# Kernel optimization log

Measured on AMD Instinct MI355X. Metric: run time of the kernel, lower is better.

Reference implementation:

```python
import jax, jax.numpy as jnp
import numpy as np

N_NODES = 100000

def graph_conv(x, src, dst, W_rel, W_root, b, num_nodes):
    # PyG GraphConv: out_i = lin_rel(sum_{j in N(i)} x_j) + lin_root(x_i)
    agg = jax.ops.segment_sum(x[src], dst, num_segments=num_nodes)  # [N, F_in]
    return agg @ W_rel + x @ W_root + b


def setup_inputs() -> dict:
    key = jax.random.key(0)
    ks = jax.random.split(key, 8)
    z = jax.random.normal(ks[0], (N_NODES, 64), dtype=jnp.float32)
    edge_index = jax.random.randint(ks[1], (2, 1600000), 0, N_NODES, dtype=jnp.int64)
    def glorot(k, fi, fo):
        s = (6.0 / (fi + fo)) ** 0.5
        return jax.random.uniform(k, (fi, fo), dtype=jnp.float32, minval=-s, maxval=s)
    return {
        "z": z,
        "edge_index": edge_index,
        "W_rel1": glorot(ks[2], 64, 32), "W_root1": glorot(ks[3], 64, 32), "b1": jnp.zeros((32,), jnp.float32),
        "W_rel2": glorot(ks[4], 32, 16), "W_root2": glorot(ks[5], 32, 16), "b2": jnp.zeros((16,), jnp.float32),
        "W_rel3": glorot(ks[6], 16, 2), "W_root3": glorot(ks[7], 16, 2), "b3": jnp.zeros((2,), jnp.float32),
    }


def reference(z, edge_index, W_rel1, W_root1, b1, W_rel2, W_root2, b2, W_rel3, W_root3, b3):
    src, dst = edge_index[0], edge_index[1]
    h = graph_conv(z, src, dst, W_rel1, W_root1, b1, N_NODES)
    h = jax.nn.relu(h)
    h = graph_conv(h, src, dst, W_rel2, W_root2, b2, N_NODES)
    h = jax.nn.relu(h)
    h = graph_conv(h, src, dst, W_rel3, W_root3, b3, N_NODES)
    return jax.nn.softmax(h, axis=-1)
```

## Files before the change

kernel.cpp:

```cpp
#include <hip/hip_runtime.h>


#define RNODES 128
#define NB_MAX 1024
#define CH 4096
#define CMAX 512

template <int Fin, int Fout, bool RELU>
__global__ void linear_q2_kernel(const float* __restrict__ x,
                                 const float* __restrict__ Wrel,
                                 const float* __restrict__ Wroot,
                                 const float* __restrict__ bias,
                                 short* __restrict__ t,
                                 float* __restrict__ tscale,
                                 float* __restrict__ acc, int N) {
    const bool rootTask = (blockIdx.y != 0);
    const float* __restrict__ W = rootTask ? Wroot : Wrel;

    int n = blockIdx.x * blockDim.x + threadIdx.x;
    if (n >= N) return;

    float o[Fout];
#pragma unroll
    for (int f = 0; f < Fout; ++f) o[f] = 0.f;

    const float* xr = x + (size_t)n * Fin;
#pragma unroll
    for (int k = 0; k < Fin; k += 4) {
        float4 v = *(const float4*)(xr + k);
        if (RELU) {
            v.x = fmaxf(v.x, 0.f); v.y = fmaxf(v.y, 0.f);
            v.z = fmaxf(v.z, 0.f); v.w = fmaxf(v.w, 0.f);
        }
        const float xv[4] = {v.x, v.y, v.z, v.w};
#pragma unroll
        for (int kk = 0; kk < 4; ++kk) {
            const float* wr = W + (size_t)(k + kk) * Fout;
#pragma unroll
            for (int f = 0; f < Fout; ++f)
                o[f] = fmaf(xv[kk], wr[f], o[f]);
        }
    }

    if (rootTask) {
#pragma unroll
        for (int f = 0; f < Fout; ++f) o[f] += bias[f];
        float* arow = acc + (size_t)n * Fout;
        if constexpr (Fout >= 4) {
#pragma unroll
            for (int f = 0; f < Fout; f += 4)
                *(float4*)(arow + f) = make_float4(o[f], o[f+1], o[f+2], o[f+3]);
        } else {
            *(float2*)arow = make_float2(o[0], o[1]);
        }
    } else {
        float m = 0.f;
#pragma unroll
        for (int f = 0; f < Fout; ++f) m = fmaxf(m, fabsf(o[f]));
        const float inv = (m > 0.f) ? (32767.0f / m) : 0.f;
        tscale[n] = m * (1.0f / 32767.0f);

        short q[Fout];
#pragma unroll
        for (int f = 0; f < Fout; ++f) q[f] = (short)__float2int_rn(o[f] * inv);

        short* trow = t + (size_t)n * Fout;
        if constexpr (Fout >= 8) {
#pragma unroll
            for (int f = 0; f < Fout; f += 8)
                *(int4*)(trow + f) = *(const int4*)(q + f);
        } else {
            *(int*)trow = (int)(unsigned short)q[0] | ((int)q[1] << 16);
        }
    }
}

template <int Fin, int Fout, bool RELU>
__global__ void linear2_kernel(const float* __restrict__ x,
                               const float* __restrict__ Wrel,
                               const float* __restrict__ Wroot,
                               const float* __restrict__ bias,
                               float* __restrict__ t,
                               float* __restrict__ acc, int N) {
    const bool rootTask = (blockIdx.y != 0);
    const float* __restrict__ W = rootTask ? Wroot : Wrel;
    float* __restrict__ outp    = rootTask ? acc : t;

    int n = blockIdx.x * blockDim.x + threadIdx.x;
    if (n >= N) return;

    float o[Fout];
#pragma unroll
    for (int f = 0; f < Fout; ++f) o[f] = 0.f;

    const float* xr = x + (size_t)n * Fin;
#pragma unroll
    for (int k = 0; k < Fin; k += 4) {
        float4 v = *(const float4*)(xr + k);
        if (RELU) {
            v.x = fmaxf(v.x, 0.f); v.y = fmaxf(v.y, 0.f);
            v.z = fmaxf(v.z, 0.f); v.w = fmaxf(v.w, 0.f);
        }
        const float xv[4] = {v.x, v.y, v.z, v.w};
#pragma unroll
        for (int kk = 0; kk < 4; ++kk) {
            const float* wr = W + (size_t)(k + kk) * Fout;
#pragma unroll
            for (int f = 0; f < Fout; ++f)
                o[f] = fmaf(xv[kk], wr[f], o[f]);
        }
    }
    if (rootTask) {
#pragma unroll
        for (int f = 0; f < Fout; ++f) o[f] += bias[f];
    }
    float* op = outp + (size_t)n * Fout;
    if constexpr (Fout >= 4) {
#pragma unroll
        for (int f = 0; f < Fout; f += 4)
            *(float4*)(op + f) = make_float4(o[f], o[f + 1], o[f + 2], o[f + 3]);
    } else {
        *(float2*)op = make_float2(o[0], o[1]);
    }
}

__global__ void hist_chunked_kernel(const int* __restrict__ dst,
                                    int* __restrict__ chunkhist,
                                    int nE, int NB) {
    __shared__ int h[NB_MAX];
    const int c  = blockIdx.x;
    const int e0 = c * CH, e1 = min(e0 + CH, nE);
    for (int b = threadIdx.x; b < NB; b += blockDim.x) h[b] = 0;
    __syncthreads();
    for (int e = e0 + threadIdx.x; e < e1; e += blockDim.x)
        atomicAdd(&h[dst[e] >> 7], 1);
    __syncthreads();
    for (int b = threadIdx.x; b < NB; b += blockDim.x)
        chunkhist[(size_t)c * NB + b] = h[b];
}

__global__ void scan_chunkhist_kernel(int* __restrict__ chunkhist,
                                      int* __restrict__ gtotal,
                                      int C, int NB) {
    __shared__ int s[CMAX];
    const int b = blockIdx.x;
    const int t = threadIdx.x;
    int v = (t < C) ? chunkhist[(size_t)t * NB + b] : 0;
    s[t] = v;
    __syncthreads();
    for (int off = 1; off < CMAX; off <<= 1) {
        int u = (t >= off) ? s[t - off] : 0;
        __syncthreads();
        s[t] += u;
        __syncthreads();
    }
    if (t < C) chunkhist[(size_t)t * NB + b] = s[t] - v;
    if (t == CMAX - 1) gtotal[b] = s[t];
}

__global__ void scan_buckets_kernel(const int* __restrict__ gtotal,
                                    int* __restrict__ bptr, int NB, int nE) {
    __shared__ int s[NB_MAX];
    int t = threadIdx.x;
    int own = (t < NB) ? gtotal[t] : 0;
    s[t] = own;
    __syncthreads();
    for (int off = 1; off < NB_MAX; off <<= 1) {
        int v = (t >= off) ? s[t - off] : 0;
        __syncthreads();
        s[t] += v;
        __syncthreads();
    }
    if (t < NB) bptr[t] = s[t] - own;
    if (t == 0) bptr[NB] = nE;
}

__global__ void bucketize_det_kernel(const int* __restrict__ src,
                                     const int* __restrict__ dst,
                                     const int* __restrict__ chunkpre,
                                     const int* __restrict__ bptr,
                                     unsigned int* __restrict__ records,
                                     int nE, int NB) {
    __shared__ int lcur[NB_MAX];
    const int c  = blockIdx.x;
    const int e0 = c * CH, e1 = min(e0 + CH, nE);
    for (int b = threadIdx.x; b < NB; b += blockDim.x)
        lcur[b] = bptr[b] + chunkpre[(size_t)c * NB + b];
    __syncthreads();
    for (int e = e0 + threadIdx.x; e < e1; e += blockDim.x) {
        int d = dst[e];
        int b = d >> 7;
        int pos = atomicAdd(&lcur[b], 1);
        records[pos] = (unsigned int)src[e] | ((unsigned int)(d & 127) << 17);
    }
}

__global__ void place_merge_kernel(const unsigned int* __restrict__ records,
                                   const int* __restrict__ bptr,
                                   int* __restrict__ rowptr,
                                   int* __restrict__ srcs_sorted,
                                   int N, int nE, int NB) {
    __shared__ int hist[RNODES];
    __shared__ int s[RNODES];
    __shared__ int lcur[RNODES];
    const int b    = blockIdx.x;
    const int base = b * RNODES;
    const int nn   = min(RNODES, N - base);
    const int beg  = bptr[b], end = bptr[b + 1];
    const int t    = threadIdx.x;

    if (t < RNODES) hist[t] = 0;
    __syncthreads();
    for (int i = beg + t; i < end; i += blockDim.x)
        atomicAdd(&hist[records[i] >> 17], 1);
    __syncthreads();

    if (t < RNODES) s[t] = hist[t];
    __syncthreads();
    for (int off = 1; off < RNODES; off <<= 1) {
        int v = (t < RNODES && t >= off) ? s[t - off] : 0;
        __syncthreads();
        if (t < RNODES && t >= off) s[t] += v;
        __syncthreads();
    }
    if (t < nn) {
        int ex = beg + s[t] - hist[t];
        rowptr[base + t] = ex;
        lcur[t] = ex;
    }
    if (b == NB - 1 && t == 0) rowptr[N] = nE;
    __syncthreads();

    for (int i = beg + t; i < end; i += blockDim.x) {
        unsigned int rec = records[i];
        int pos = atomicAdd(&lcur[rec >> 17], 1);
        srcs_sorted[pos] = (int)(rec & 0x1FFFFu);
    }
}

template <int F, bool SOFTMAX>
__global__ void gather_agg_q_kernel(const short* __restrict__ t,
                                    const float* __restrict__ tscale,
                                    const int* __restrict__ rowptr,
                                    const int* __restrict__ srcs,
                                    const float* __restrict__ rootacc,
                                    float* __restrict__ out, int N) {
    constexpr int P = (F >= 4) ? (F / 2) : 1;
    constexpr int S = F / 2;
    int tid = blockIdx.x * blockDim.x + threadIdx.x;
    int n  = (P == 1) ? tid : (tid / P);
    int fp = (P == 1) ? 0   : (tid & (P - 1));
    if (n >= N) return;

    const int* tp = (const int*)t;
    int beg = rowptr[n], end = rowptr[n + 1];
    float sx = 0.f, sy = 0.f;
    int e = beg;
    for (; e + 8 <= end; e += 8) {
        int s[8];
#pragma unroll
        for (int u = 0; u < 8; ++u) s[u] = srcs[e + u];
        int q[8]; float sc[8];
#pragma unroll
        for (int u = 0; u < 8; ++u) {
            q[u]  = tp[s[u] * S + fp];
            sc[u] = tscale[s[u]];
        }
#pragma unroll
        for (int u = 0; u < 8; ++u) {
            float lo = (float)((short)(q[u] & 0xFFFF));
            float hi = (float)(q[u] >> 16);
            sx = fmaf(sc[u], lo, sx);
            sy = fmaf(sc[u], hi, sy);
        }
    }
    for (; e < end; ++e) {
        int s0 = srcs[e];
        int qv = tp[s0 * S + fp];
        float sc = tscale[s0];
        sx = fmaf(sc, (float)((short)(qv & 0xFFFF)), sx);
        sy = fmaf(sc, (float)(qv >> 16), sy);
    }

    const float2 r0 = *(const float2*)(rootacc + (size_t)n * F + 2 * fp);
    float a = r0.x + sx, b = r0.y + sy;
    if (!SOFTMAX) {
        *(float2*)(out + (size_t)n * F + 2 * fp) = make_float2(a, b);
    } else {
        float m = fmaxf(a, b);
        float ea = __expf(a - m), eb = __expf(b - m);
        float inv = 1.0f / (ea + eb);
        *(float2*)(out + (size_t)n * 2) = make_float2(ea * inv, eb * inv);
    }
}

template <int F>
__global__ void scatter_kernel(const float* __restrict__ t,
                               const int* __restrict__ src,
                               const int* __restrict__ dst,
                               float* __restrict__ acc, int nE) {
    int tid = blockIdx.x * blockDim.x + threadIdx.x;
    int e = tid / F;
    if (e >= nE) return;
    int f = tid & (F - 1);
    atomicAdd(acc + (long)dst[e] * F + f, t[(long)src[e] * F + f]);
}

__global__ void softmax2_kernel(const float* __restrict__ h, float* __restrict__ out, int N) {
    int n = blockIdx.x * blockDim.x + threadIdx.x;
    if (n >= N) return;
    float a = h[2 * n], b = h[2 * n + 1];
    float m = fmaxf(a, b);
    float ea = __expf(a - m), eb = __expf(b - m);
    float inv = 1.0f / (ea + eb);
    out[2 * n] = ea * inv;
    out[2 * n + 1] = eb * inv;
}

extern "C" void kernel_launch(void* const* d_in, const int* in_sizes, int n_in,
                              void* d_out, int out_size, void* d_ws, size_t ws_size,
                              hipStream_t stream) {
    const float* z      = (const float*)d_in[0];
    const int*   ei     = (const int*)d_in[1];
    const float* Wrel1  = (const float*)d_in[2];
    const float* Wroot1 = (const float*)d_in[3];
    const float* b1     = (const float*)d_in[4];
    const float* Wrel2  = (const float*)d_in[5];
    const float* Wroot2 = (const float*)d_in[6];
    const float* b2     = (const float*)d_in[7];
    const float* Wrel3  = (const float*)d_in[8];
    const float* Wroot3 = (const float*)d_in[9];
    const float* b3     = (const float*)d_in[10];

    const int N  = in_sizes[0] / 64;
    const int nE = in_sizes[1] / 2;
    const int* src = ei;
    const int* dst = ei + nE;
    const int NB = (N + RNODES - 1) / RNODES;
    const int C  = (nE + CH - 1) / CH;

    char* wsb = (char*)d_ws;
    size_t off = 0;
    auto take = [&](size_t bytes) -> void* {
        void* p = (void*)(wsb + off);
        off = (off + bytes + 255) & ~(size_t)255;
        return p;
    };
    int*          chunkhist   = (int*)take((size_t)CMAX * NB_MAX * 4);
    int*          gtotal      = (int*)take((size_t)NB_MAX * 4);
    int*          bptr        = (int*)take((size_t)(NB_MAX + 1) * 4);
    unsigned int* records     = (unsigned int*)take((size_t)nE * 4);
    int*          rowptr      = (int*)take((size_t)(N + 1) * 4);
    int*          srcs_sorted = (int*)take((size_t)nE * 4);
    short*        t1          = (short*)take((size_t)N * 32 * 2);
    float*        s1          = (float*)take((size_t)N * 4);
    float*        h1          = (float*)take((size_t)N * 32 * 4);
    short*        t2          = (short*)take((size_t)N * 16 * 2);
    float*        s2          = (float*)take((size_t)N * 4);
    float*        h2          = (float*)take((size_t)N * 16 * 4);
    short*        t3          = (short*)take((size_t)N * 2 * 2);
    float*        s3          = (float*)take((size_t)N * 4);
    float*        h3          = (float*)take((size_t)N * 2 * 4);
    const size_t needed = off;

    const int B = 256;
    const int nodeBlocks = (N + B - 1) / B;
    const dim3 linGrid(nodeBlocks, 2);
    const bool packOK = (N <= (1 << 17)) && (NB <= NB_MAX) && (C <= CMAX);

    if (ws_size >= needed && packOK) {
        hist_chunked_kernel<<<C, 512, 0, stream>>>(dst, chunkhist, nE, NB);
        scan_chunkhist_kernel<<<NB, CMAX, 0, stream>>>(chunkhist, gtotal, C, NB);
        scan_buckets_kernel<<<1, NB_MAX, 0, stream>>>(gtotal, bptr, NB, nE);
        bucketize_det_kernel<<<C, 512, 0, stream>>>(src, dst, chunkhist, bptr, records, nE, NB);
        place_merge_kernel<<<NB, 512, 0, stream>>>(records, bptr, rowptr, srcs_sorted, N, nE, NB);

        linear_q2_kernel<64, 32, false><<<linGrid, B, 0, stream>>>(
            z, Wrel1, Wroot1, b1, t1, s1, h1, N);
        gather_agg_q_kernel<32, false><<<((size_t)N * 16 + B - 1) / B, B, 0, stream>>>(
            t1, s1, rowptr, srcs_sorted, h1, h1, N);

        linear_q2_kernel<32, 16, true><<<linGrid, B, 0, stream>>>(
            h1, Wrel2, Wroot2, b2, t2, s2, h2, N);
        gather_agg_q_kernel<16, false><<<((size_t)N * 8 + B - 1) / B, B, 0, stream>>>(
            t2, s2, rowptr, srcs_sorted, h2, h2, N);

        linear_q2_kernel<16, 2, true><<<linGrid, B, 0, stream>>>(
            h2, Wrel3, Wroot3, b3, t3, s3, h3, N);
        gather_agg_q_kernel<2, true><<<((size_t)N + B - 1) / B, B, 0, stream>>>(
            t3, s3, rowptr, srcs_sorted, h3, (float*)d_out, N);
    } else {
        float* regionA = (float*)d_ws;
        float* regionB = regionA + (size_t)N * 32;
        float* ft1 = regionA;
        float* fh1 = regionB;
        float* ft2 = regionA;
        float* fh2 = regionA + (size_t)N * 16;
        float* ft3 = regionB;
        float* fh3 = regionB + (size_t)N * 2;
        linear2_kernel<64, 32, false><<<linGrid, B, 0, stream>>>(z, Wrel1, Wroot1, b1, ft1, fh1, N);
        scatter_kernel<32><<<((size_t)nE * 32 + B - 1) / B, B, 0, stream>>>(ft1, src, dst, fh1, nE);
        linear2_kernel<32, 16, true><<<linGrid, B, 0, stream>>>(fh1, Wrel2, Wroot2, b2, ft2, fh2, N);
        scatter_kernel<16><<<((size_t)nE * 16 + B - 1) / B, B, 0, stream>>>(ft2, src, dst, fh2, nE);
        linear2_kernel<16, 2, true><<<linGrid, B, 0, stream>>>(fh2, Wrel3, Wroot3, b3, ft3, fh3, N);
        scatter_kernel<2><<<((size_t)nE * 2 + B - 1) / B, B, 0, stream>>>(ft3, src, dst, fh3, nE);
        softmax2_kernel<<<nodeBlocks, B, 0, stream>>>(fh3, (float*)d_out, N);
    }
}
```

Baseline: 248.1 us.

## Inline quantization scale into gathered rows for layers 2 and 3

```diff
diff --git a/kernel.cpp b/kernel.cpp
--- a/kernel.cpp
+++ b/kernel.cpp
@@ -58,19 +58,28 @@
 #pragma unroll
         for (int f = 0; f < Fout; ++f) m = fmaxf(m, fabsf(o[f]));
         const float inv = (m > 0.f) ? (32767.0f / m) : 0.f;
-        tscale[n] = m * (1.0f / 32767.0f);
+        const float sc  = m * (1.0f / 32767.0f);
 
         short q[Fout];
 #pragma unroll
         for (int f = 0; f < Fout; ++f) q[f] = (short)__float2int_rn(o[f] * inv);
 
-        short* trow = t + (size_t)n * Fout;
-        if constexpr (Fout >= 8) {
-#pragma unroll
-            for (int f = 0; f < Fout; f += 8)
+        if constexpr (Fout == 32) {
+            tscale[n] = sc;
+            short* trow = t + (size_t)n * 32;
+#pragma unroll
+            for (int f = 0; f < 32; f += 8)
                 *(int4*)(trow + f) = *(const int4*)(q + f);
+        } else if constexpr (Fout == 16) {
+            short* trow = t + (size_t)n * 32;
+            *(int4*)(trow)     = *(const int4*)(q);
+            *(int4*)(trow + 8) = *(const int4*)(q + 8);
+            ((float*)trow)[8]  = sc;
         } else {
-            *(int*)trow = (int)(unsigned short)q[0] | ((int)q[1] << 16);
+            int2 r;
+            r.x = (int)(unsigned short)q[0] | ((int)q[1] << 16);
+            r.y = __float_as_int(sc);
+            *(int2*)(t + (size_t)n * 4) = r;
         }
     }
 }
@@ -287,6 +296,93 @@
     if (!SOFTMAX) {
         *(float2*)(out + (size_t)n * F + 2 * fp) = make_float2(a, b);
     } else {
+        float m = fmaxf(a, b);
+        float ea = __expf(a - m), eb = __expf(b - m);
+        float inv = 1.0f / (ea + eb);
+        *(float2*)(out + (size_t)n * 2) = make_float2(ea * inv, eb * inv);
+    }
+}
+
+__global__ void gather16_inl_kernel(const short* __restrict__ t,
+                                    const int* __restrict__ rowptr,
+                                    const int* __restrict__ srcs,
+                                    const float* __restrict__ rootacc,
+                                    float* __restrict__ out, int N) {
+    int tid = blockIdx.x * blockDim.x + threadIdx.x;
+    int n  = tid >> 3;
+    int fp = tid & 7;
+    if (n >= N) return;
+
+    const int* tp = (const int*)t;
+    int beg = rowptr[n], end = rowptr[n + 1];
+    float sx = 0.f, sy = 0.f;
+    int e = beg;
+    for (; e + 8 <= end; e += 8) {
+        int s[8];
+#pragma unroll
+        for (int u = 0; u < 8; ++u) s[u] = srcs[e + u];
+        int q[8]; float sc[8];
+#pragma unroll
+        for (int u = 0; u < 8; ++u) {
+            const int* row = tp + (size_t)s[u] * 16;
+            q[u]  = row[fp];
+            sc[u] = __int_as_float(row[8]);
+        }
+#pragma unroll
+        for (int u = 0; u < 8; ++u) {
+            sx = fmaf(sc[u], (float)((short)(q[u] & 0xFFFF)), sx);
+            sy = fmaf(sc[u], (float)(q[u] >> 16), sy);
+        }
+    }
+    for (; e < end; ++e) {
+        const int* row = tp + (size_t)srcs[e] * 16;
+        int qv = row[fp];
+        float sc = __int_as_float(row[8]);
+        sx = fmaf(sc, (float)((short)(qv & 0xFFFF)), sx);
+        sy = fmaf(sc, (float)(qv >> 16), sy);
+    }
+
+    const float2 r0 = *(const float2*)(rootacc + (size_t)n * 16 + 2 * fp);
+    *(float2*)(out + (size_t)n * 16 + 2 * fp) = make_float2(r0.x + sx, r0.y + sy);
+}
+
+__global__ void gather2_inl_kernel(const short* __restrict__ t,
+                                   const int* __restrict__ rowptr,
+                                   const int* __restrict__ srcs,
+                                   const float* __restrict__ rootacc,
+                                   float* __restrict__ out, int N) {
+    int tid = blockIdx.x * blockDim.x + threadIdx.x;
+    int n  = tid >> 2;
+    int fp = tid & 3;
+    if (n >= N) return;
+
+    const int2* tp = (const int2*)t;
+    int beg = rowptr[n], end = rowptr[n + 1];
+    float sx = 0.f, sy = 0.f;
+    int e = beg + fp;
+    for (; e + 12 < end; e += 16) {
+        int s0 = srcs[e], s1 = srcs[e + 4], s2 = srcs[e + 8], s3 = srcs[e + 12];
+        int2 r0 = tp[s0], r1 = tp[s1], r2 = tp[s2], r3 = tp[s3];
+        sx = fmaf(__int_as_float(r0.y), (float)((short)(r0.x & 0xFFFF)), sx);
+        sy = fmaf(__int_as_float(r0.y), (float)(r0.x >> 16), sy);
+        sx = fmaf(__int_as_float(r1.y), (float)((short)(r1.x & 0xFFFF)), sx);
+        sy = fmaf(__int_as_float(r1.y), (float)(r1.x >> 16), sy);
+        sx = fmaf(__int_as_float(r2.y), (float)((short)(r2.x & 0xFFFF)), sx);
+        sy = fmaf(__int_as_float(r2.y), (float)(r2.x >> 16), sy);
+        sx = fmaf(__int_as_float(r3.y), (float)((short)(r3.x & 0xFFFF)), sx);
+        sy = fmaf(__int_as_float(r3.y), (float)(r3.x >> 16), sy);
+    }
+    for (; e < end; e += 4) {
+        int2 r = tp[srcs[e]];
+        sx = fmaf(__int_as_float(r.y), (float)((short)(r.x & 0xFFFF)), sx);
+        sy = fmaf(__int_as_float(r.y), (float)(r.x >> 16), sy);
+    }
+    sx += __shfl_xor(sx, 1, 64); sy += __shfl_xor(sy, 1, 64);
+    sx += __shfl_xor(sx, 2, 64); sy += __shfl_xor(sy, 2, 64);
+
+    if (fp == 0) {
+        const float2 r0 = *(const float2*)(rootacc + (size_t)n * 2);
+        float a = r0.x + sx, b = r0.y + sy;
         float m = fmaxf(a, b);
         float ea = __expf(a - m), eb = __expf(b - m);
         float inv = 1.0f / (ea + eb);
@@ -355,11 +451,9 @@
     short*        t1          = (short*)take((size_t)N * 32 * 2);
     float*        s1          = (float*)take((size_t)N * 4);
     float*        h1          = (float*)take((size_t)N * 32 * 4);
-    short*        t2          = (short*)take((size_t)N * 16 * 2);
-    float*        s2          = (float*)take((size_t)N * 4);
+    short*        t2          = (short*)take((size_t)N * 64);
     float*        h2          = (float*)take((size_t)N * 16 * 4);
-    short*        t3          = (short*)take((size_t)N * 2 * 2);
-    float*        s3          = (float*)take((size_t)N * 4);
+    short*        t3          = (short*)take((size_t)N * 8);
     float*        h3          = (float*)take((size_t)N * 2 * 4);
     const size_t needed = off;
 
@@ -381,14 +475,14 @@
             t1, s1, rowptr, srcs_sorted, h1, h1, N);
 
         linear_q2_kernel<32, 16, true><<<linGrid, B, 0, stream>>>(
-            h1, Wrel2, Wroot2, b2, t2, s2, h2, N);
-        gather_agg_q_kernel<16, false><<<((size_t)N * 8 + B - 1) / B, B, 0, stream>>>(
-            t2, s2, rowptr, srcs_sorted, h2, h2, N);
+            h1, Wrel2, Wroot2, b2, t2, nullptr, h2, N);
+        gather16_inl_kernel<<<((size_t)N * 8 + B - 1) / B, B, 0, stream>>>(
+            t2, rowptr, srcs_sorted, h2, h2, N);
 
         linear_q2_kernel<16, 2, true><<<linGrid, B, 0, stream>>>(
-            h2, Wrel3, Wroot3, b3, t3, s3, h3, N);
-        gather_agg_q_kernel<2, true><<<((size_t)N + B - 1) / B, B, 0, stream>>>(
-            t3, s3, rowptr, srcs_sorted, h3, (float*)d_out, N);
+            h2, Wrel3, Wroot3, b3, t3, nullptr, h3, N);
+        gather2_inl_kernel<<<((size_t)N * 4 + B - 1) / B, B, 0, stream>>>(
+            t3, rowptr, srcs_sorted, h3, (float*)d_out, N);
     } else {
         float* regionA = (float*)d_ws;
         float* regionB = regionA + (size_t)N * 32;
```

After: 243.0 us. -2.0%, faster.

## Aggregate directly from dst-bucketed records with shared-memory atomics, drop CSR build

Applied to the files above, without the earlier changes.

```diff
diff --git a/kernel.cpp b/kernel.cpp
--- a/kernel.cpp
+++ b/kernel.cpp
@@ -58,19 +58,28 @@
 #pragma unroll
         for (int f = 0; f < Fout; ++f) m = fmaxf(m, fabsf(o[f]));
         const float inv = (m > 0.f) ? (32767.0f / m) : 0.f;
-        tscale[n] = m * (1.0f / 32767.0f);
+        const float sc  = m * (1.0f / 32767.0f);
 
         short q[Fout];
 #pragma unroll
         for (int f = 0; f < Fout; ++f) q[f] = (short)__float2int_rn(o[f] * inv);
 
-        short* trow = t + (size_t)n * Fout;
-        if constexpr (Fout >= 8) {
-#pragma unroll
-            for (int f = 0; f < Fout; f += 8)
+        if constexpr (Fout == 32) {
+            tscale[n] = sc;
+            short* trow = t + (size_t)n * 32;
+#pragma unroll
+            for (int f = 0; f < 32; f += 8)
                 *(int4*)(trow + f) = *(const int4*)(q + f);
+        } else if constexpr (Fout == 16) {
+            short* trow = t + (size_t)n * 32;
+            *(int4*)(trow)     = *(const int4*)(q);
+            *(int4*)(trow + 8) = *(const int4*)(q + 8);
+            ((float*)trow)[8]  = sc;
         } else {
-            *(int*)trow = (int)(unsigned short)q[0] | ((int)q[1] << 16);
+            int2 r;
+            r.x = (int)(unsigned short)q[0] | ((int)q[1] << 16);
+            r.y = __float_as_int(sc);
+            *(int2*)(t + (size_t)n * 4) = r;
         }
     }
 }
@@ -195,102 +204,80 @@
     }
 }
 
-__global__ void place_merge_kernel(const unsigned int* __restrict__ records,
-                                   const int* __restrict__ bptr,
-                                   int* __restrict__ rowptr,
-                                   int* __restrict__ srcs_sorted,
-                                   int N, int nE, int NB) {
-    __shared__ int hist[RNODES];
-    __shared__ int s[RNODES];
-    __shared__ int lcur[RNODES];
+template <int F, bool SOFTMAX>
+__global__ void bucket_gather_kernel(const short* __restrict__ t,
+                                     const float* __restrict__ tscale,
+                                     const unsigned int* __restrict__ records,
+                                     const int* __restrict__ bptr,
+                                     const float* __restrict__ rootacc,
+                                     float* __restrict__ out, int N) {
+    __shared__ float accs[RNODES * (F + 1)];
     const int b    = blockIdx.x;
     const int base = b * RNODES;
     const int nn   = min(RNODES, N - base);
     const int beg  = bptr[b], end = bptr[b + 1];
-    const int t    = threadIdx.x;
-
-    if (t < RNODES) hist[t] = 0;
-    __syncthreads();
-    for (int i = beg + t; i < end; i += blockDim.x)
-        atomicAdd(&hist[records[i] >> 17], 1);
-    __syncthreads();
-
-    if (t < RNODES) s[t] = hist[t];
-    __syncthreads();
-    for (int off = 1; off < RNODES; off <<= 1) {
-        int v = (t < RNODES && t >= off) ? s[t - off] : 0;
-        __syncthreads();
-        if (t < RNODES && t >= off) s[t] += v;
-        __syncthreads();
-    }
-    if (t < nn) {
-        int ex = beg + s[t] - hist[t];
-        rowptr[base + t] = ex;
-        lcur[t] = ex;
-    }
-    if (b == NB - 1 && t == 0) rowptr[N] = nE;
-    __syncthreads();
-
-    for (int i = beg + t; i < end; i += blockDim.x) {
-        unsigned int rec = records[i];
-        int pos = atomicAdd(&lcur[rec >> 17], 1);
-        srcs_sorted[pos] = (int)(rec & 0x1FFFFu);
-    }
-}
-
-template <int F, bool SOFTMAX>
-__global__ void gather_agg_q_kernel(const short* __restrict__ t,
-                                    const float* __restrict__ tscale,
-                                    const int* __restrict__ rowptr,
-                                    const int* __restrict__ srcs,
-                                    const float* __restrict__ rootacc,
-                                    float* __restrict__ out, int N) {
-    constexpr int P = (F >= 4) ? (F / 2) : 1;
-    constexpr int S = F / 2;
-    int tid = blockIdx.x * blockDim.x + threadIdx.x;
-    int n  = (P == 1) ? tid : (tid / P);
-    int fp = (P == 1) ? 0   : (tid & (P - 1));
-    if (n >= N) return;
-
-    const int* tp = (const int*)t;
-    int beg = rowptr[n], end = rowptr[n + 1];
-    float sx = 0.f, sy = 0.f;
-    int e = beg;
-    for (; e + 8 <= end; e += 8) {
-        int s[8];
-#pragma unroll
-        for (int u = 0; u < 8; ++u) s[u] = srcs[e + u];
-        int q[8]; float sc[8];
-#pragma unroll
-        for (int u = 0; u < 8; ++u) {
-            q[u]  = tp[s[u] * S + fp];
-            sc[u] = tscale[s[u]];
-        }
-#pragma unroll
-        for (int u = 0; u < 8; ++u) {
-            float lo = (float)((short)(q[u] & 0xFFFF));
-            float hi = (float)(q[u] >> 16);
-            sx = fmaf(sc[u], lo, sx);
-            sy = fmaf(sc[u], hi, sy);
-        }
-    }
-    for (; e < end; ++e) {
-        int s0 = srcs[e];
-        int qv = tp[s0 * S + fp];
-        float sc = tscale[s0];
-        sx = fmaf(sc, (float)((short)(qv & 0xFFFF)), sx);
-        sy = fmaf(sc, (float)(qv >> 16), sy);
-    }
-
-    const float2 r0 = *(const float2*)(rootacc + (size_t)n * F + 2 * fp);
-    float a = r0.x + sx, b = r0.y + sy;
-    if (!SOFTMAX) {
-        *(float2*)(out + (size_t)n * F + 2 * fp) = make_float2(a, b);
-    } else {
-        float m = fmaxf(a, b);
-        float ea = __expf(a - m), eb = __expf(b - m);
-        float inv = 1.0f / (ea + eb);
-        *(float2*)(out + (size_t)n * 2) = make_float2(ea * inv, eb * inv);
+    const int tid  = threadIdx.x;
+
+    for (int i = tid; i < RNODES * (F + 1); i += blockDim.x) accs[i] = 0.f;
+    __syncthreads();
+
+    if constexpr (F >= 4) {
+        constexpr int LPE = F / 2;
+        const int epi = blockDim.x / LPE;
+        const int le  = tid / LPE;
+        const int fp  = tid % LPE;
+        for (int e = beg + le; e < end; e += epi) {
+            unsigned int rec = records[e];
+            int s = (int)(rec & 0x1FFFFu);
+            int d = (int)(rec >> 17);
+            float lo, hi, sc;
+            if constexpr (F == 32) {
+                int qv = ((const int*)t)[(size_t)s * 16 + fp];
+                sc = tscale[s];
+                lo = (float)((short)(qv & 0xFFFF));
+                hi = (float)(qv >> 16);
+            } else {
+                const int* row = (const int*)t + (size_t)s * 16;
+                int qv = row[fp];
+                sc = __int_as_float(row[8]);
+                lo = (float)((short)(qv & 0xFFFF));
+                hi = (float)(qv >> 16);
+            }
+            float* ar = accs + d * (F + 1) + 2 * fp;
+            atomicAdd(ar,     sc * lo);
+            atomicAdd(ar + 1, sc * hi);
+        }
+    } else {
+        for (int e = beg + tid; e < end; e += blockDim.x) {
+            unsigned int rec = records[e];
+            int s = (int)(rec & 0x1FFFFu);
+            int d = (int)(rec >> 17);
+            int2 r = ((const int2*)t)[s];
+            float sc = __int_as_float(r.y);
+            float* ar = accs + d * 3;
+            atomicAdd(ar,     sc * (float)((short)(r.x & 0xFFFF)));
+            atomicAdd(ar + 1, sc * (float)(r.x >> 16));
+        }
+    }
+    __syncthreads();
+
+    if constexpr (!SOFTMAX) {
+        for (int i = tid; i < nn * F; i += blockDim.x) {
+            int node = i / F, f = i % F;
+            float v = rootacc[(size_t)(base + node) * F + f]
+                    + accs[node * (F + 1) + f];
+            out[(size_t)(base + node) * F + f] = v;
+        }
+    } else {
+        for (int node = tid; node < nn; node += blockDim.x) {
+            const float2 r0 = *(const float2*)(rootacc + (size_t)(base + node) * 2);
+            float a = r0.x + accs[node * 3];
+            float bb = r0.y + accs[node * 3 + 1];
+            float m = fmaxf(a, bb);
+            float ea = __expf(a - m), eb = __expf(bb - m);
+            float inv = 1.0f / (ea + eb);
+            *(float2*)(out + (size_t)(base + node) * 2) = make_float2(ea * inv, eb * inv);
+        }
     }
 }
 
@@ -350,16 +337,12 @@
     int*          gtotal      = (int*)take((size_t)NB_MAX * 4);
     int*          bptr        = (int*)take((size_t)(NB_MAX + 1) * 4);
     unsigned int* records     = (unsigned int*)take((size_t)nE * 4);
-    int*          rowptr      = (int*)take((size_t)(N + 1) * 4);
-    int*          srcs_sorted = (int*)take((size_t)nE * 4);
     short*        t1          = (short*)take((size_t)N * 32 * 2);
     float*        s1          = (float*)take((size_t)N * 4);
     float*        h1          = (float*)take((size_t)N * 32 * 4);
-    short*        t2          = (short*)take((size_t)N * 16 * 2);
-    float*        s2          = (float*)take((size_t)N * 4);
+    short*        t2          = (short*)take((size_t)N * 64);
     float*        h2          = (float*)take((size_t)N * 16 * 4);
-    short*        t3          = (short*)take((size_t)N * 2 * 2);
-    float*        s3          = (float*)take((size_t)N * 4);
+    short*        t3          = (short*)take((size_t)N * 8);
     float*        h3          = (float*)take((size_t)N * 2 * 4);
     const size_t needed = off;
 
@@ -373,22 +356,21 @@
         scan_chunkhist_kernel<<<NB, CMAX, 0, stream>>>(chunkhist, gtotal, C, NB);
         scan_buckets_kernel<<<1, NB_MAX, 0, stream>>>(gtotal, bptr, NB, nE);
         bucketize_det_kernel<<<C, 512, 0, stream>>>(src, dst, chunkhist, bptr, records, nE, NB);
-        place_merge_kernel<<<NB, 512, 0, stream>>>(records, bptr, rowptr, srcs_sorted, N, nE, NB);
 
         linear_q2_kernel<64, 32, false><<<linGrid, B, 0, stream>>>(
             z, Wrel1, Wroot1, b1, t1, s1, h1, N);
-        gather_agg_q_kernel<32, false><<<((size_t)N * 16 + B - 1) / B, B, 0, stream>>>(
-            t1, s1, rowptr, srcs_sorted, h1, h1, N);
+        bucket_gather_kernel<32, false><<<NB, 512, 0, stream>>>(
+            t1, s1, records, bptr, h1, h1, N);
 
         linear_q2_kernel<32, 16, true><<<linGrid, B, 0, stream>>>(
-            h1, Wrel2, Wroot2, b2, t2, s2, h2, N);
-        gather_agg_q_kernel<16, false><<<((size_t)N * 8 + B - 1) / B, B, 0, stream>>>(
-            t2, s2, rowptr, srcs_sorted, h2, h2, N);
+            h1, Wrel2, Wroot2, b2, t2, nullptr, h2, N);
+        bucket_gather_kernel<16, false><<<NB, 512, 0, stream>>>(
+            t2, nullptr, records, bptr, h2, h2, N);
 
         linear_q2_kernel<16, 2, true><<<linGrid, B, 0, stream>>>(
-            h2, Wrel3, Wroot3, b3, t3, s3, h3, N);
-        gather_agg_q_kernel<2, true><<<((size_t)N + B - 1) / B, B, 0, stream>>>(
-            t3, s3, rowptr, srcs_sorted, h3, (float*)d_out, N);
+            h2, Wrel3, Wroot3, b3, t3, nullptr, h3, N);
+        bucket_gather_kernel<2, true><<<NB, 512, 0, stream>>>(
+            t3, nullptr, records, bptr, h3, (float*)d_out, N);
     } else {
         float* regionA = (float*)d_ws;
         float* regionB = regionA + (size_t)N * 32;
```

After: 700.0 us. 182% more time.
